# Optimization experiments

Measured on AMD Instinct MI355X. Metric: run time of the kernel, lower is better.

## Reference

```python
import jax, jax.numpy as jnp
import numpy as np

D_MODEL = 1024
N_HEAD = 16


def setup_inputs() -> dict:
    key = jax.random.key(0)
    k1, k2, k3 = jax.random.split(key, 3)
    scale = 1.0 / np.sqrt(D_MODEL)
    x = jax.random.normal(k1, (1, 4096, D_MODEL), dtype=jnp.float32)
    # nn.Linear weights stored as [out, in]; applied as x @ W.T
    w_attn = jax.random.normal(k2, (3 * D_MODEL, D_MODEL), dtype=jnp.float32) * scale
    w_proj = jax.random.normal(k3, (D_MODEL, D_MODEL), dtype=jnp.float32) * scale
    return {"x": x, "w_attn": w_attn, "w_proj": w_proj}


def reference(x, w_attn, w_proj):
    B, T, C = x.shape
    H = N_HEAD
    hd = C // H
    qkv = x @ w_attn.T                      # [B, T, 3C]
    q, k, v = jnp.split(qkv, 3, axis=-1)
    # [B, T, C] -> [B, H, T, hd]
    q = q.reshape(B, T, H, hd).transpose(0, 2, 1, 3)
    k = k.reshape(B, T, H, hd).transpose(0, 2, 1, 3)
    v = v.reshape(B, T, H, hd).transpose(0, 2, 1, 3)
    att = jnp.einsum("bhqd,bhkd->bhqk", q, k) * (1.0 / np.sqrt(hd))  # [B,H,T,T]
    causal = jnp.tril(jnp.ones((T, T), dtype=bool))
    att = jnp.where(causal[None, None], att, -jnp.inf)
    att = jax.nn.softmax(att, axis=-1)
    y = jnp.einsum("bhqk,bhkd->bhqd", att, v)  # [B,H,T,hd]
    y = y.transpose(0, 2, 1, 3).reshape(B, T, C)
    return y @ w_proj.T
```

## Files before the change

### kernel.cpp

```cpp
#include <hip/hip_runtime.h>
#include <hip/hip_bf16.h>
#include <stdint.h>

typedef __bf16 bf16x8 __attribute__((ext_vector_type(8)));
typedef float f32x4 __attribute__((ext_vector_type(4)));

#define T_SEQ 4096
#define C_DIM 1024
#define H_NUM 16
#define HD 64
#define C3 3072
#define NEG_BIG (-30000.0f)

__device__ __forceinline__ unsigned short f2bf(float f) {
    uint32_t u = __builtin_bit_cast(uint32_t, f);
    u += 0x7fffu + ((u >> 16) & 1u);
    return (unsigned short)(u >> 16);
}

__device__ __forceinline__ uint32_t pk_bf16(float a, float b) {
    __hip_bfloat162 h = __float22bfloat162_rn(float2{a, b});
    uint32_t u;
    __builtin_memcpy(&u, &h, sizeof(u));
    return u;
}

__device__ __forceinline__ bf16x8 ld_bf8(const unsigned short* p) {
    return *reinterpret_cast<const bf16x8*>(p);
}

__device__ __forceinline__ void async_g2l16(const unsigned short* g, unsigned short* l) {
    __builtin_amdgcn_global_load_lds(
        (const __attribute__((address_space(1))) void*)g,
        (__attribute__((address_space(3))) void*)l, 16, 0, 0);
}

__device__ __forceinline__ void store_c(unsigned short* C, size_t idx, float v) { C[idx] = f2bf(v); }
__device__ __forceinline__ void store_c(float* C, size_t idx, float v)          { C[idx] = v; }

__device__ __forceinline__ void cvt8(const float* src, unsigned short* dst) {
    float4 f0 = *(const float4*)src;
    float4 f1 = *(const float4*)(src + 4);
    union { uint32_t w[4]; uint4 q; } t;
    t.w[0] = pk_bf16(f0.x, f0.y);
    t.w[1] = pk_bf16(f0.z, f0.w);
    t.w[2] = pk_bf16(f1.x, f1.y);
    t.w[3] = pk_bf16(f1.z, f1.w);
    *(uint4*)dst = t.q;
}

__global__ void cvt_all(const float* __restrict__ x, const float* __restrict__ wa,
                        const float* __restrict__ wp,
                        unsigned short* __restrict__ xb, unsigned short* __restrict__ wab,
                        unsigned short* __restrict__ wpb) {
    int i = (blockIdx.x * blockDim.x + threadIdx.x) * 8;
    if (i < T_SEQ * C_DIM) { cvt8(x + i, xb + i); return; }
    i -= T_SEQ * C_DIM;
    if (i < C3 * C_DIM) { cvt8(wa + i, wab + i); return; }
    i -= C3 * C_DIM;
    if (wpb != nullptr && i < C_DIM * C_DIM) cvt8(wp + i, wpb + i);
}

__global__ void cvt_f32_bf16(const float* __restrict__ src, unsigned short* __restrict__ dst, int n) {
    int i = (blockIdx.x * blockDim.x + threadIdx.x) * 8;
    if (i >= n) return;
    cvt8(src + i, dst + i);
}

template <int BM, typename TC>
__global__ __launch_bounds__(BM * 2, (BM == 128) ? 2 : 3) void gemm_bt(
    const unsigned short* __restrict__ A, const unsigned short* __restrict__ B,
    TC* __restrict__ C, unsigned short* __restrict__ VT, int M, int N, int K)
{
    __shared__ __attribute__((aligned(16))) unsigned short As[BM * 32];
    __shared__ __attribute__((aligned(16))) unsigned short Bs[128 * 32];

    const int tid  = threadIdx.x;
    const int wave = tid >> 6, lane = tid & 63;
    const int quad = lane >> 4, l16 = lane & 15;
    const int wm = (BM == 128) ? (wave >> 1) : 0;
    const int wn = (BM == 128) ? (wave & 1) : wave;
    const int m0 = blockIdx.y * BM, n0 = blockIdx.x * 128;

    const int sr   = lane >> 2;
    const int scol = (lane & 3) * 8;

    f32x4 acc[4][4] = {};

    for (int k0 = 0; k0 < K; k0 += 32) {
        if constexpr (BM == 128) {
            const unsigned short* ga = A + (size_t)(m0 + wave * 32 + sr) * K + k0 + scol;
            const unsigned short* gb = B + (size_t)(n0 + wave * 32 + sr) * K + k0 + scol;
            unsigned short* la = As + (wave * 32) * 32;
            unsigned short* lb = Bs + (wave * 32) * 32;
            async_g2l16(ga, la);
            async_g2l16(ga + (size_t)16 * K, la + 16 * 32);
            async_g2l16(gb, lb);
            async_g2l16(gb + (size_t)16 * K, lb + 16 * 32);
        } else {
            const unsigned short* ga = A + (size_t)(m0 + wave * 32 + sr) * K + k0 + scol;
            unsigned short* la = As + (wave * 32) * 32;
            async_g2l16(ga, la);
            async_g2l16(ga + (size_t)16 * K, la + 16 * 32);
            const unsigned short* gb = B + (size_t)(n0 + wave * 64 + sr) * K + k0 + scol;
            unsigned short* lb = Bs + (wave * 64) * 32;
            async_g2l16(gb, lb);
            async_g2l16(gb + (size_t)16 * K, lb + 16 * 32);
            async_g2l16(gb + (size_t)32 * K, lb + 32 * 32);
            async_g2l16(gb + (size_t)48 * K, lb + 48 * 32);
        }
        __syncthreads();

        bf16x8 af[4], bf[4];
        #pragma unroll
        for (int i = 0; i < 4; ++i) {
            af[i] = ld_bf8(As + (wm * 64 + i * 16 + l16) * 32 + quad * 8);
            bf[i] = ld_bf8(Bs + (wn * 64 + i * 16 + l16) * 32 + quad * 8);
        }
        #pragma unroll
        for (int mt = 0; mt < 4; ++mt)
            #pragma unroll
            for (int nt = 0; nt < 4; ++nt)
                acc[mt][nt] = __builtin_amdgcn_mfma_f32_16x16x32_bf16(
                    af[mt], bf[nt], acc[mt][nt], 0, 0, 0);
        __syncthreads();
    }

    if (VT != nullptr && n0 >= 2 * C_DIM) {
        #pragma unroll
        for (int mt = 0; mt < 4; ++mt)
            #pragma unroll
            for (int nt = 0; nt < 4; ++nt) {
                const int ch = n0 - 2 * C_DIM + wn * 64 + nt * 16 + l16;
                const int t0 = m0 + wm * 64 + mt * 16 + quad * 4;
                union { unsigned short u[4]; uint2 q; } pk;
                #pragma unroll
                for (int r = 0; r < 4; ++r) pk.u[r] = f2bf(acc[mt][nt][r]);
                *(uint2*)(VT + (size_t)ch * T_SEQ + t0) = pk.q;
            }
    } else {
        #pragma unroll
        for (int mt = 0; mt < 4; ++mt)
            #pragma unroll
            for (int nt = 0; nt < 4; ++nt)
                #pragma unroll
                for (int r = 0; r < 4; ++r) {
                    int row = m0 + wm * 64 + mt * 16 + quad * 4 + r;
                    int col = n0 + wn * 64 + nt * 16 + l16;
                    store_c(C, (size_t)row * N + col, acc[mt][nt][r]);
                }
    }
}

#if __has_builtin(__builtin_amdgcn_permlane32_swap) && __has_builtin(__builtin_amdgcn_permlane16_swap)
#define HAVE_PERMLANE_SWAP 1
#else
#define HAVE_PERMLANE_SWAP 0
#endif

__device__ __forceinline__ void quad_xpose_pair(uint32_t X, uint32_t Y,
                                                uint32_t& t0, uint32_t& t1) {
#if HAVE_PERMLANE_SWAP
    auto S = __builtin_amdgcn_permlane32_swap((int)X, (int)Y, false, false);
    auto T = __builtin_amdgcn_permlane16_swap((int)S[0], (int)S[1], false, false);
    t0 = (uint32_t)T[0];
    t1 = (uint32_t)T[1];
#else
    const unsigned l = threadIdx.x & 63;
    uint32_t Ys = (uint32_t)__shfl_xor((int)Y, 32, 64);
    uint32_t Xs = (uint32_t)__shfl_xor((int)X, 32, 64);
    uint32_t S0 = (l < 32) ? X : Ys;
    uint32_t S1 = (l < 32) ? Xs : Y;
    uint32_t S0s = (uint32_t)__shfl_xor((int)S0, 16, 64);
    uint32_t S1s = (uint32_t)__shfl_xor((int)S1, 16, 64);
    t0 = (l & 16) ? S1s : S0;
    t1 = (l & 16) ? S1 : S0s;
#endif
}

template <bool MASK>
__device__ __forceinline__ void fa7_tile(
    const unsigned short* Ksb, const unsigned short* Vsb,
    const bf16x8 qf[2][2], f32x4 o[2][4], float* l_part,
    int k0, int q_abs0, int quad, int l16, int fo0, int fo1)
{
    const unsigned short* krow = Ksb + l16 * 64;
    bf16x8 kf[4][2];
    #pragma unroll
    for (int s = 0; s < 4; ++s) {
        kf[s][0] = ld_bf8(krow + s * 1024 + fo0);
        kf[s][1] = ld_bf8(krow + s * 1024 + fo1);
    }

    bf16x8 pf[2][2];
    #pragma unroll
    for (int qs = 0; qs < 2; ++qs) {
        f32x4 st[4];
        __builtin_amdgcn_s_setprio(1);
        #pragma unroll
        for (int s = 0; s < 4; ++s) {
            f32x4 z = {};
            z = __builtin_amdgcn_mfma_f32_16x16x32_bf16(kf[s][0], qf[qs][0], z, 0, 0, 0);
            st[s] = __builtin_amdgcn_mfma_f32_16x16x32_bf16(kf[s][1], qf[qs][1], z, 0, 0, 0);
        }
        __builtin_amdgcn_s_setprio(0);

        float ts = 0.f;
        #pragma unroll
        for (int s = 0; s < 4; ++s)
            #pragma unroll
            for (int r = 0; r < 4; ++r) {
                float v = st[s][r];
                if (MASK) {
                    int key = k0 + s * 16 + quad * 4 + r;
                    v = (key <= q_abs0 + qs * 16) ? v : NEG_BIG;
                }
                float e = __builtin_amdgcn_exp2f(v);
                st[s][r] = e;
                ts += e;
            }
        l_part[qs] += ts;

        uint32_t W[4][2];
        #pragma unroll
        for (int s = 0; s < 4; ++s) {
            W[s][0] = pk_bf16(st[s][0], st[s][1]);
            W[s][1] = pk_bf16(st[s][2], st[s][3]);
        }
        union { uint32_t w[4]; bf16x8 v; } pA, pB;
        quad_xpose_pair(W[0][0], W[1][0], pA.w[0], pA.w[2]);
        quad_xpose_pair(W[0][1], W[1][1], pA.w[1], pA.w[3]);
        quad_xpose_pair(W[2][0], W[3][0], pB.w[0], pB.w[2]);
        quad_xpose_pair(W[2][1], W[3][1], pB.w[1], pB.w[3]);
        pf[qs][0] = pA.v;
        pf[qs][1] = pB.v;
    }

    const unsigned short* vrow = Vsb + l16 * 64;
    bf16x8 vf[4][2];
    #pragma unroll
    for (int c = 0; c < 4; ++c) {
        vf[c][0] = ld_bf8(vrow + c * 1024 + fo0);
        vf[c][1] = ld_bf8(vrow + c * 1024 + fo1);
    }
    __builtin_amdgcn_s_setprio(1);
    #pragma unroll
    for (int qs = 0; qs < 2; ++qs)
        #pragma unroll
        for (int c = 0; c < 4; ++c) {
            o[qs][c] = __builtin_amdgcn_mfma_f32_16x16x32_bf16(vf[c][0], pf[qs][0], o[qs][c], 0, 0, 0);
            o[qs][c] = __builtin_amdgcn_mfma_f32_16x16x32_bf16(vf[c][1], pf[qs][1], o[qs][c], 0, 0, 0);
        }
    __builtin_amdgcn_s_setprio(0);
}

__global__ __launch_bounds__(512, 2) void flash_attn11(
    const unsigned short* __restrict__ qkv,
    const unsigned short* __restrict__ Vt,
    unsigned short* __restrict__ Y)
{
    __shared__ __attribute__((aligned(16))) unsigned short Ks[2][2][4096];
    __shared__ __attribute__((aligned(16))) unsigned short Vs[2][2][4096];

    const int tid  = threadIdx.x;
    const int wave = tid >> 6, lane = tid & 63;
    const int quad = lane >> 4, l16 = lane & 15;
    const int wq = wave >> 1, wk = wave & 1;

    const int bi  = blockIdx.x;
    const int gen = bi >> 8, s = bi & 255;
    const int h   = s & 15;
    const int idx = s >> 4;
    const int j   = (gen == 0) ? (31 - idx) : idx;

    const int q0w    = j * 128 + wq * 32;
    const int q_abs0 = q0w + l16;
    const int sw  = l16 & 7;
    const int fo0 = (quad ^ sw) * 8;
    const int fo1 = ((quad + 4) ^ sw) * 8;

    bf16x8 qf[2][2];
    {
        const float QS = 0.125f * 1.44269504f;
        #pragma unroll
        for (int qs = 0; qs < 2; ++qs) {
            const unsigned short* qp =
                qkv + (size_t)(q0w + qs * 16 + l16) * C3 + h * HD + quad * 8;
            bf16x8 a = ld_bf8(qp), b = ld_bf8(qp + 32);
            #pragma unroll
            for (int i = 0; i < 8; ++i) {
                qf[qs][0][i] = (__bf16)((float)a[i] * QS);
                qf[qs][1][i] = (__bf16)((float)b[i] * QS);
            }
        }
    }

    const int tt = wave >> 1, hf = wave & 1;
    const int srow   = lane >> 3;
    const int schunk = (lane & 7) ^ srow;
    const unsigned short* gp;
    size_t gstep, rstep;
    unsigned short* lbase;
    if (tt < 2) {
        gp = qkv + (size_t)(tt * 64 + hf * 32 + srow) * C3 + C_DIM + h * HD + schunk * 8;
        gstep = (size_t)8 * C3;
        rstep = (size_t)128 * C3;
        lbase = &Ks[0][tt][(hf * 32) * 64];
    } else {
        const int vt = tt - 2;
        gp = Vt + (size_t)(h * HD + hf * 32 + srow) * T_SEQ + vt * 64 + schunk * 8;
        gstep = (size_t)8 * T_SEQ;
        rstep = (size_t)128;
        lbase = &Vs[0][vt][(hf * 32) * 64];
    }
    const int lds_db = 2 * 4096;

    auto stage = [&](int b) {
        #pragma unroll
        for (int jj = 0; jj < 4; ++jj)
            async_g2l16(gp + jj * gstep, lbase + b * lds_db + jj * 8 * 64);
    };

    f32x4 o[2][4] = {};
    float l_part[2] = {0.f, 0.f};

    const int nt = 2 * (j + 1);
    const int R  = j + 1;
    stage(0);
    gp += rstep;

    for (int r = 0; r < R; ++r) {
        __syncthreads();
        const int b = r & 1;
        if (r + 1 < R) {
            stage(1 - b);
            gp += rstep;
        }
        const int t = 2 * r + wk;
        if (t < nt && t * 64 <= q0w + 31) {
            if (t * 64 + 63 <= q0w)
                fa7_tile<false>(&Ks[b][wk][0], &Vs[b][wk][0], qf, o, l_part,
                                t * 64, q_abs0, quad, l16, fo0, fo1);
            else
                fa7_tile<true>(&Ks[b][wk][0], &Vs[b][wk][0], qf, o, l_part,
                               t * 64, q_abs0, quad, l16, fo0, fo1);
        }
    }

    __syncthreads();
    float* red  = (float*)&Ks[0][0][0];
    float* lred = (float*)&Vs[0][0][0];
    if (wk == 1) {
        #pragma unroll
        for (int qs = 0; qs < 2; ++qs)
            #pragma unroll
            for (int c = 0; c < 4; ++c)
                *(f32x4*)&red[((wq * 8 + qs * 4 + c) * 64 + lane) * 4] = o[qs][c];
        lred[wq * 128 + lane * 2 + 0] = l_part[0];
        lred[wq * 128 + lane * 2 + 1] = l_part[1];
    }
    __syncthreads();
    if (wk == 0) {
        #pragma unroll
        for (int qs = 0; qs < 2; ++qs) {
            #pragma unroll
            for (int c = 0; c < 4; ++c) {
                f32x4 p = *(f32x4*)&red[((wq * 8 + qs * 4 + c) * 64 + lane) * 4];
                o[qs][c] += p;
            }
            l_part[qs] += lred[wq * 128 + lane * 2 + qs];
        }

        #pragma unroll
        for (int qs = 0; qs < 2; ++qs) {
            float l = l_part[qs];
            l += __shfl_xor(l, 16, 64);
            l += __shfl_xor(l, 32, 64);
            float inv_l = 1.f / l;
            #pragma unroll
            for (int c = 0; c < 4; ++c) {
                union { uint32_t w[2]; uint2 q; } t;
                t.w[0] = pk_bf16(o[qs][c][0] * inv_l, o[qs][c][1] * inv_l);
                t.w[1] = pk_bf16(o[qs][c][2] * inv_l, o[qs][c][3] * inv_l);
                *(uint2*)(Y + (size_t)(q_abs0 + qs * 16) * C_DIM + h * HD + c * 16 + quad * 4) = t.q;
            }
        }
    }
}

extern "C" void kernel_launch(void* const* d_in, const int* in_sizes, int n_in,
                              void* d_out, int out_size, void* d_ws, size_t ws_size,
                              hipStream_t stream) {
    const float* x      = (const float*)d_in[0];
    const float* w_attn = (const float*)d_in[1];
    const float* w_proj = (const float*)d_in[2];
    float* out = (float*)d_out;

    unsigned short* qkv = (unsigned short*)d_ws;
    unsigned short* xb  = qkv + (size_t)T_SEQ * C3;
    unsigned short* y   = xb;
    unsigned short* Vt  = (unsigned short*)d_out;
    unsigned short* wab = Vt + (size_t)C_DIM * T_SEQ;

    const size_t need = ((size_t)T_SEQ * C3 + (size_t)T_SEQ * C_DIM +
                         (size_t)C_DIM * C_DIM) * sizeof(unsigned short);
    const bool fuse_wp = ws_size >= need;
    unsigned short* wpb = fuse_wp ? (xb + (size_t)T_SEQ * C_DIM)
                                  : qkv;

    if (fuse_wp) {
        const int n8 = (T_SEQ * C_DIM + C3 * C_DIM + C_DIM * C_DIM) / 8;
        cvt_all<<<n8 / 256, 256, 0, stream>>>(x, w_attn, w_proj, xb, wab, wpb);
    } else {
        const int n8 = (T_SEQ * C_DIM + C3 * C_DIM) / 8;
        cvt_all<<<n8 / 256, 256, 0, stream>>>(x, w_attn, nullptr, xb, wab, nullptr);
    }

    gemm_bt<128, unsigned short>
        <<<dim3(C3 / 128, T_SEQ / 128), 256, 0, stream>>>(xb, wab, qkv, Vt, T_SEQ, C3, C_DIM);

    flash_attn11<<<dim3(512), 512, 0, stream>>>(qkv, Vt, y);

    if (!fuse_wp) {
        cvt_f32_bf16<<<(C_DIM * C_DIM / 8 + 255) / 256, 256, 0, stream>>>(w_proj, wpb, C_DIM * C_DIM);
    }

    gemm_bt<64, float>
        <<<dim3(C_DIM / 128, T_SEQ / 64), 128, 0, stream>>>(y, wpb, out, nullptr, T_SEQ, C_DIM, C_DIM);
}
```

Measured before the change: 203.0 us.

## Split flash attention into 64-query blocks with intra-tile key split across waves

Reworks the attention kernel from 512 blocks of 8 waves covering 128 queries into 1024 blocks of 4 waves covering 64 queries. Each pair of waves now splits every 64-key tile into two 32-key halves instead of alternating whole tiles. The aim is finer causal load balancing, less wasted masked work, and higher occupancy with smaller LDS. In exchange, each block re-stages K and V tiles that the old larger blocks shared, so global and LDS traffic per query rises, and there are more barriers per unit of work.

```diff
diff --git a/kernel.cpp b/kernel.cpp
--- a/kernel.cpp
+++ b/kernel.cpp
@@ -179,26 +179,27 @@
 }
 
 template <bool MASK>
-__device__ __forceinline__ void fa7_tile(
+__device__ __forceinline__ void fa12_tile(
     const unsigned short* Ksb, const unsigned short* Vsb,
     const bf16x8 qf[2][2], f32x4 o[2][4], float* l_part,
-    int k0, int q_abs0, int quad, int l16, int fo0, int fo1)
+    int k0, int q_abs0, int quad, int l16, int wk, int fo0, int fo1)
 {
-    const unsigned short* krow = Ksb + l16 * 64;
-    bf16x8 kf[4][2];
+    const int fos = wk ? fo1 : fo0;
+    bf16x8 kf[2][2];
     #pragma unroll
-    for (int s = 0; s < 4; ++s) {
-        kf[s][0] = ld_bf8(krow + s * 1024 + fo0);
-        kf[s][1] = ld_bf8(krow + s * 1024 + fo1);
-    }
-
-    bf16x8 pf[2][2];
+    for (int s = 0; s < 2; ++s) {
+        const unsigned short* krow = Ksb + (wk * 32 + s * 16 + l16) * 64;
+        kf[s][0] = ld_bf8(krow + fo0);
+        kf[s][1] = ld_bf8(krow + fo1);
+    }
+
+    bf16x8 pf[2];
     #pragma unroll
     for (int qs = 0; qs < 2; ++qs) {
-        f32x4 st[4];
+        f32x4 st[2];
         __builtin_amdgcn_s_setprio(1);
         #pragma unroll
-        for (int s = 0; s < 4; ++s) {
+        for (int s = 0; s < 2; ++s) {
             f32x4 z = {};
             z = __builtin_amdgcn_mfma_f32_16x16x32_bf16(kf[s][0], qf[qs][0], z, 0, 0, 0);
             st[s] = __builtin_amdgcn_mfma_f32_16x16x32_bf16(kf[s][1], qf[qs][1], z, 0, 0, 0);
@@ -207,7 +208,7 @@
 
         float ts = 0.f;
         #pragma unroll
-        for (int s = 0; s < 4; ++s)
+        for (int s = 0; s < 2; ++s)
             #pragma unroll
             for (int r = 0; r < 4; ++r) {
                 float v = st[s][r];
@@ -221,59 +222,49 @@
             }
         l_part[qs] += ts;
 
-        uint32_t W[4][2];
-        #pragma unroll
-        for (int s = 0; s < 4; ++s) {
+        uint32_t W[2][2];
+        #pragma unroll
+        for (int s = 0; s < 2; ++s) {
             W[s][0] = pk_bf16(st[s][0], st[s][1]);
             W[s][1] = pk_bf16(st[s][2], st[s][3]);
         }
-        union { uint32_t w[4]; bf16x8 v; } pA, pB;
+        union { uint32_t w[4]; bf16x8 v; } pA;
         quad_xpose_pair(W[0][0], W[1][0], pA.w[0], pA.w[2]);
         quad_xpose_pair(W[0][1], W[1][1], pA.w[1], pA.w[3]);
-        quad_xpose_pair(W[2][0], W[3][0], pB.w[0], pB.w[2]);
-        quad_xpose_pair(W[2][1], W[3][1], pB.w[1], pB.w[3]);
-        pf[qs][0] = pA.v;
-        pf[qs][1] = pB.v;
-    }
-
-    const unsigned short* vrow = Vsb + l16 * 64;
-    bf16x8 vf[4][2];
+        pf[qs] = pA.v;
+    }
+
+    bf16x8 vf[4];
     #pragma unroll
-    for (int c = 0; c < 4; ++c) {
-        vf[c][0] = ld_bf8(vrow + c * 1024 + fo0);
-        vf[c][1] = ld_bf8(vrow + c * 1024 + fo1);
-    }
+    for (int c = 0; c < 4; ++c)
+        vf[c] = ld_bf8(Vsb + (c * 16 + l16) * 64 + fos);
     __builtin_amdgcn_s_setprio(1);
     #pragma unroll
     for (int qs = 0; qs < 2; ++qs)
         #pragma unroll
-        for (int c = 0; c < 4; ++c) {
-            o[qs][c] = __builtin_amdgcn_mfma_f32_16x16x32_bf16(vf[c][0], pf[qs][0], o[qs][c], 0, 0, 0);
-            o[qs][c] = __builtin_amdgcn_mfma_f32_16x16x32_bf16(vf[c][1], pf[qs][1], o[qs][c], 0, 0, 0);
-        }
+        for (int c = 0; c < 4; ++c)
+            o[qs][c] = __builtin_amdgcn_mfma_f32_16x16x32_bf16(vf[c], pf[qs], o[qs][c], 0, 0, 0);
     __builtin_amdgcn_s_setprio(0);
 }
 
-__global__ __launch_bounds__(512, 2) void flash_attn11(
+__global__ __launch_bounds__(256, 4) void flash_attn12(
     const unsigned short* __restrict__ qkv,
     const unsigned short* __restrict__ Vt,
     unsigned short* __restrict__ Y)
 {
-    __shared__ __attribute__((aligned(16))) unsigned short Ks[2][2][4096];
-    __shared__ __attribute__((aligned(16))) unsigned short Vs[2][2][4096];
+    __shared__ __attribute__((aligned(16))) unsigned short Ks[2][4096];
+    __shared__ __attribute__((aligned(16))) unsigned short Vs[2][4096];
 
     const int tid  = threadIdx.x;
     const int wave = tid >> 6, lane = tid & 63;
     const int quad = lane >> 4, l16 = lane & 15;
     const int wq = wave >> 1, wk = wave & 1;
 
-    const int bi  = blockIdx.x;
-    const int gen = bi >> 8, s = bi & 255;
-    const int h   = s & 15;
-    const int idx = s >> 4;
-    const int j   = (gen == 0) ? (31 - idx) : idx;
-
-    const int q0w    = j * 128 + wq * 32;
+    const int bi = blockIdx.x;
+    const int h  = bi & 15;
+    const int qb = (bi < 512) ? (63 - (bi >> 4)) : (31 - ((bi - 512) >> 4));
+
+    const int q0w    = qb * 64 + wq * 32;
     const int q_abs0 = q0w + l16;
     const int sw  = l16 & 7;
     const int fo0 = (quad ^ sw) * 8;
@@ -301,55 +292,49 @@
     const unsigned short* gp;
     size_t gstep, rstep;
     unsigned short* lbase;
-    if (tt < 2) {
-        gp = qkv + (size_t)(tt * 64 + hf * 32 + srow) * C3 + C_DIM + h * HD + schunk * 8;
+    if (tt == 0) {
+        gp = qkv + (size_t)(hf * 32 + srow) * C3 + C_DIM + h * HD + schunk * 8;
         gstep = (size_t)8 * C3;
-        rstep = (size_t)128 * C3;
-        lbase = &Ks[0][tt][(hf * 32) * 64];
+        rstep = (size_t)64 * C3;
+        lbase = &Ks[0][(hf * 32) * 64];
     } else {
-        const int vt = tt - 2;
-        gp = Vt + (size_t)(h * HD + hf * 32 + srow) * T_SEQ + vt * 64 + schunk * 8;
+        gp = Vt + (size_t)(h * HD + hf * 32 + srow) * T_SEQ + schunk * 8;
         gstep = (size_t)8 * T_SEQ;
-        rstep = (size_t)128;
-        lbase = &Vs[0][vt][(hf * 32) * 64];
-    }
-    const int lds_db = 2 * 4096;
+        rstep = (size_t)64;
+        lbase = &Vs[0][(hf * 32) * 64];
+    }
 
     auto stage = [&](int b) {
         #pragma unroll
         for (int jj = 0; jj < 4; ++jj)
-            async_g2l16(gp + jj * gstep, lbase + b * lds_db + jj * 8 * 64);
+            async_g2l16(gp + jj * gstep, lbase + b * 4096 + jj * 8 * 64);
     };
 
     f32x4 o[2][4] = {};
     float l_part[2] = {0.f, 0.f};
 
-    const int nt = 2 * (j + 1);
-    const int R  = j + 1;
+    const int nt = qb + 1;
     stage(0);
     gp += rstep;
 
-    for (int r = 0; r < R; ++r) {
+    for (int t = 0; t < nt; ++t) {
         __syncthreads();
-        const int b = r & 1;
-        if (r + 1 < R) {
+        const int b = t & 1;
+        if (t + 1 < nt) {
             stage(1 - b);
             gp += rstep;
         }
-        const int t = 2 * r + wk;
-        if (t < nt && t * 64 <= q0w + 31) {
-            if (t * 64 + 63 <= q0w)
-                fa7_tile<false>(&Ks[b][wk][0], &Vs[b][wk][0], qf, o, l_part,
-                                t * 64, q_abs0, quad, l16, fo0, fo1);
-            else
-                fa7_tile<true>(&Ks[b][wk][0], &Vs[b][wk][0], qf, o, l_part,
-                               t * 64, q_abs0, quad, l16, fo0, fo1);
-        }
+        if (t == nt - 1)
+            fa12_tile<true>(Ks[b], Vs[b], qf, o, l_part,
+                            t * 64 + wk * 32, q_abs0, quad, l16, wk, fo0, fo1);
+        else
+            fa12_tile<false>(Ks[b], Vs[b], qf, o, l_part,
+                             t * 64 + wk * 32, q_abs0, quad, l16, wk, fo0, fo1);
     }
 
     __syncthreads();
-    float* red  = (float*)&Ks[0][0][0];
-    float* lred = (float*)&Vs[0][0][0];
+    float* red  = (float*)&Ks[0][0];
+    float* lred = (float*)&Vs[0][0];
     if (wk == 1) {
         #pragma unroll
         for (int qs = 0; qs < 2; ++qs)
@@ -419,7 +404,7 @@
     gemm_bt<128, unsigned short>
         <<<dim3(C3 / 128, T_SEQ / 128), 256, 0, stream>>>(xb, wab, qkv, Vt, T_SEQ, C3, C_DIM);
 
-    flash_attn11<<<dim3(512), 512, 0, stream>>>(qkv, Vt, y);
+    flash_attn12<<<dim3(1024), 256, 0, stream>>>(qkv, Vt, y);
 
     if (!fuse_wp) {
         cvt_f32_bf16<<<(C_DIM * C_DIM / 8 + 255) / 256, 256, 0, stream>>>(w_proj, wpb, C_DIM * C_DIM);
```

Result: faster. 188.8 us (median of 4 runs) (-7.0%).
